# Performance work log

Hardware: AMD Instinct MI355X
Metric: run time of the kernel (lower is better)

Reference implementation:

```python
import jax, jax.numpy as jnp
import numpy as np

B, E, N, D = 4, 16, 1024, 512

def setup_inputs() -> dict:
    key = jax.random.key(0)
    kx, k1, k2, k3 = jax.random.split(key, 4)
    std = 1.0 / np.sqrt(D)
    x = jax.random.normal(kx, (B, E, N, D), dtype=jnp.float32)
    # weights: uniform(-std, std) per init_
    w1 = jax.random.uniform(k1, (E, D, D), dtype=jnp.float32, minval=-std, maxval=std)
    w2 = jax.random.uniform(k2, (E, D, D), dtype=jnp.float32, minval=-std, maxval=std)
    w3 = jax.random.uniform(k3, (E, D, D), dtype=jnp.float32, minval=-std, maxval=std)
    return {"x": x, "w1": w1, "w2": w2, "w3": w3}

def reference(x, w1, w2, w3):
    # per-expert projections: [b,e,n,d] x [e,d,h] -> [b,e,n,h]
    q = jnp.einsum('bend,edh->benh', x, w1)
    k = jnp.einsum('bend,edh->benh', x, w2)
    v = jnp.einsum('bend,edh->benh', x, w3)
    # global (n-reduced) attention: [b,e,h,d]
    atten = jnp.einsum('benh,bend->behd', q, k)
    atten = jax.nn.softmax(atten, axis=-1)
    # [b,e,n,h] x [b,e,h,h] -> [b,e,n,h]
    out = jnp.einsum('benh,behd->bend', v, atten)
    return out
```

## Files before the change

kernel.cpp:

```cpp
#include <hip/hip_runtime.h>
#include <stdint.h>

typedef unsigned short u16;
typedef __attribute__((ext_vector_type(8))) short bf16x8;
typedef __attribute__((ext_vector_type(4))) float floatx4;
typedef __attribute__((ext_vector_type(4))) u16 u16x4;
typedef __attribute__((ext_vector_type(8))) u16 u16x8;

constexpr int B_ = 4, E_ = 16, N_ = 1024, D_ = 512;
constexpr int BE = B_ * E_;

__device__ __forceinline__ u16 f2bf(float f) {
    union { float f; uint32_t u; } v; v.f = f;
    return (u16)((v.u + 0x7fffu + ((v.u >> 16) & 1u)) >> 16);
}
__device__ __forceinline__ float bf2f(u16 h) {
    union { uint32_t u; float f; } v; v.u = ((uint32_t)h) << 16;
    return v.f;
}

#define GLDS(g, l) __builtin_amdgcn_global_load_lds( \
    (const __attribute__((address_space(1))) void*)(g), \
    (__attribute__((address_space(3))) void*)(l), 16, 0, 0)


__global__ __launch_bounds__(256)
void transpose_split(const float* __restrict__ in, u16* __restrict__ outH,
                     u16* __restrict__ outL, int R, int C)
{
    __shared__ float t[32][33];
    const int z = blockIdx.z;
    const float* ib = in + (size_t)z * R * C;
    u16* oh = outH + (size_t)z * R * C;
    u16* ol = outL + (size_t)z * R * C;
    const int r0 = blockIdx.y * 32, c0 = blockIdx.x * 32;
    const int t8 = threadIdx.x & 7, td = threadIdx.x >> 3;

    float4 v = *(const float4*)&ib[(size_t)(r0 + td) * C + c0 + t8 * 4];
    t[td][t8 * 4 + 0] = v.x;
    t[td][t8 * 4 + 1] = v.y;
    t[td][t8 * 4 + 2] = v.z;
    t[td][t8 * 4 + 3] = v.w;
    __syncthreads();

    u16x4 ph, pl;
    float w0 = t[t8 * 4 + 0][td], w1 = t[t8 * 4 + 1][td];
    float w2 = t[t8 * 4 + 2][td], w3 = t[t8 * 4 + 3][td];
    ph.x = f2bf(w0); pl.x = f2bf(w0 - bf2f(ph.x));
    ph.y = f2bf(w1); pl.y = f2bf(w1 - bf2f(ph.y));
    ph.z = f2bf(w2); pl.z = f2bf(w2 - bf2f(ph.z));
    ph.w = f2bf(w3); pl.w = f2bf(w3 - bf2f(ph.w));
    const size_t o = (size_t)(c0 + td) * R + r0 + t8 * 4;
    *(u16x4*)&oh[o] = ph;
    *(u16x4*)&ol[o] = pl;
}

__global__ __launch_bounds__(256)
void transpose_split_w(const float* __restrict__ inA, u16* __restrict__ oAh, u16* __restrict__ oAl,
                       const float* __restrict__ inB, u16* __restrict__ oBh, u16* __restrict__ oBl)
{
    __shared__ float t[32][33];
    int z = blockIdx.z;
    const float* in; u16* oh; u16* ol;
    if (z < E_) { in = inA; oh = oAh; ol = oAl; }
    else        { z -= E_; in = inB; oh = oBh; ol = oBl; }
    const int R = 512, C = 512;
    const float* ib = in + (size_t)z * R * C;
    u16* ohz = oh + (size_t)z * R * C;
    u16* olz = ol + (size_t)z * R * C;
    const int r0 = blockIdx.y * 32, c0 = blockIdx.x * 32;
    const int t8 = threadIdx.x & 7, td = threadIdx.x >> 3;

    float4 v = *(const float4*)&ib[(size_t)(r0 + td) * C + c0 + t8 * 4];
    t[td][t8 * 4 + 0] = v.x;
    t[td][t8 * 4 + 1] = v.y;
    t[td][t8 * 4 + 2] = v.z;
    t[td][t8 * 4 + 3] = v.w;
    __syncthreads();

    u16x4 ph, pl;
    float w0 = t[t8 * 4 + 0][td], w1 = t[t8 * 4 + 1][td];
    float w2 = t[t8 * 4 + 2][td], w3 = t[t8 * 4 + 3][td];
    ph.x = f2bf(w0); pl.x = f2bf(w0 - bf2f(ph.x));
    ph.y = f2bf(w1); pl.y = f2bf(w1 - bf2f(ph.y));
    ph.z = f2bf(w2); pl.z = f2bf(w2 - bf2f(ph.z));
    ph.w = f2bf(w3); pl.w = f2bf(w3 - bf2f(ph.w));
    const size_t o = (size_t)(c0 + td) * R + r0 + t8 * 4;
    *(u16x4*)&ohz[o] = ph;
    *(u16x4*)&olz[o] = pl;
}

__global__ __launch_bounds__(256)
void gemm_split3(const u16* __restrict__ Ah, const u16* __restrict__ Al,
                 int aMod, long aStride,
                 const u16* __restrict__ Bh, const u16* __restrict__ Bl,
                 int bMod, long bStride,
                 u16* __restrict__ Ch, u16* __restrict__ Cl,
                 float* __restrict__ Cf,
                 int M, int N, int K, int f32out, int sym)
{
    const int z = blockIdx.z;
    const long za = aMod ? (z % aMod) : z;
    const long zb = bMod ? (z % bMod) : z;
    const u16* pAh = Ah + za * aStride;
    const u16* pAl = Al + za * aStride;
    const u16* pBh = Bh + zb * bStride;
    const u16* pBl = Bl + zb * bStride;

    __shared__ __attribute__((aligned(16))) u16 sA[8192];
    __shared__ __attribute__((aligned(16))) u16 sB[8192];

    const int tid = threadIdx.x;
    const int wv = tid >> 6, ln = tid & 63;
    const int lq = ln >> 4, lm = ln & 15;

    int bi, bj;
    if (sym) {
        const int idx = blockIdx.x;
        bi = (idx < 4) ? 0 : (idx < 7) ? 1 : (idx < 9) ? 2 : 3;
        bj = idx - ((bi == 0) ? 0 : (bi == 1) ? 3 : (bi == 2) ? 5 : 6);
    } else { bi = blockIdx.x; bj = blockIdx.y; }
    const int m0 = bi * 128, n0 = bj * 128;

    const int rg = ln >> 2;
    const int kq = ((ln & 3) + (rg >> 1)) & 3;
    const u16* srcA[4];
    const u16* srcB[4];
#pragma unroll
    for (int g = 0; g < 4; ++g) {
        const int grp = wv * 4 + g;
        const int row = (grp >> 3) * 64 + ((grp >> 1) & 3) * 16 + rg;
        srcA[g] = ((grp & 1) ? pAl : pAh) + (long)(m0 + row) * K + kq * 8;
        srcB[g] = ((grp & 1) ? pBl : pBh) + (long)(n0 + row) * K + kq * 8;
    }

    const int co = (lm * 4 + ((lq - (lm >> 1)) & 3)) * 8;

    const int wm = wv >> 1, wn = wv & 1;

    floatx4 acc[4][4];
#pragma unroll
    for (int i = 0; i < 4; ++i)
#pragma unroll
        for (int j = 0; j < 4; ++j) acc[i][j] = (floatx4){0.f, 0.f, 0.f, 0.f};

    for (int k0 = 0; k0 < K; k0 += 32) {
#pragma unroll
        for (int g = 0; g < 4; ++g) {
            GLDS(srcA[g] + k0, sA + (wv * 4 + g) * 512);
            GLDS(srcB[g] + k0, sB + (wv * 4 + g) * 512);
        }
        __syncthreads();

        bf16x8 ah[4], al[4], bh[4], bl[4];
#pragma unroll
        for (int i = 0; i < 4; ++i) {
            const int ga = (wm * 8 + i * 2) * 512 + co;
            ah[i] = *(const bf16x8*)&sA[ga];
            al[i] = *(const bf16x8*)&sA[ga + 512];
        }
#pragma unroll
        for (int j = 0; j < 4; ++j) {
            const int gb = (wn * 8 + j * 2) * 512 + co;
            bh[j] = *(const bf16x8*)&sB[gb];
            bl[j] = *(const bf16x8*)&sB[gb + 512];
        }
#pragma unroll
        for (int i = 0; i < 4; ++i)
#pragma unroll
            for (int j = 0; j < 4; ++j) {
                acc[i][j] = __builtin_amdgcn_mfma_f32_16x16x32_bf16(ah[i], bh[j], acc[i][j], 0, 0, 0);
                acc[i][j] = __builtin_amdgcn_mfma_f32_16x16x32_bf16(ah[i], bl[j], acc[i][j], 0, 0, 0);
                acc[i][j] = __builtin_amdgcn_mfma_f32_16x16x32_bf16(al[i], bh[j], acc[i][j], 0, 0, 0);
            }
        __syncthreads();
    }

    const long cbase = (long)z * M * N;
#pragma unroll
    for (int i = 0; i < 4; ++i)
#pragma unroll
        for (int j = 0; j < 4; ++j) {
            const int col = n0 + wn * 64 + j * 16 + lm;
            const int row0 = m0 + wm * 64 + i * 16 + lq * 4;
            if (f32out) {
#pragma unroll
                for (int r = 0; r < 4; ++r)
                    Cf[cbase + (long)(row0 + r) * N + col] = acc[i][j][r];
            } else {
                u16x4 hv, lv;
#pragma unroll
                for (int r = 0; r < 4; ++r) {
                    const float v = acc[i][j][r];
                    const u16 h = f2bf(v);
                    hv[r] = h;
                    lv[r] = f2bf(v - bf2f(h));
                    Ch[cbase + (long)(row0 + r) * N + col] = h;
                    Cl[cbase + (long)(row0 + r) * N + col] = lv[r];
                }
                if (sym && bi != bj) {
                    const long mb = cbase + (long)col * N + row0;
                    *(u16x4*)&Ch[mb] = hv;
                    *(u16x4*)&Cl[mb] = lv;
                }
            }
        }
}

template<int OTFA, int F32OUT>
__global__ __launch_bounds__(256)
void gemm_plain(const float* __restrict__ Qf, int qMod, long qStride,
                const u16* __restrict__ Pb, int pMod, long pStride,
                u16* __restrict__ Cb, float* __restrict__ Cf,
                int M, int N, int K)
{
    const int z = blockIdx.z;
    const float* pQ = Qf + (long)(qMod ? z % qMod : z) * qStride;
    const u16*  pP = Pb + (long)(pMod ? z % pMod : z) * pStride;

    __shared__ __attribute__((aligned(16))) u16 sA[4096];
    __shared__ __attribute__((aligned(16))) u16 sB[4096];

    const int tid = threadIdx.x;
    const int wv = tid >> 6, ln = tid & 63;
    const int lq = ln >> 4, lm = ln & 15;
    const int m0 = blockIdx.x * 128, n0 = blockIdx.y * 128;

    u16* sBF = OTFA ? sB : sA;
    u16* sQ  = OTFA ? sA : sB;
    const int bfRow0 = OTFA ? n0 : m0;
    const int qRow0  = OTFA ? m0 : n0;

    const int rg = ln >> 2;
    const int kqr = ((ln & 3) + (rg >> 1)) & 3;
    const u16* srcP[2];
#pragma unroll
    for (int g = 0; g < 2; ++g) {
        const int grp = wv * 2 + g;
        const int row = (grp >> 2) * 64 + (grp & 3) * 16 + rg;
        srcP[g] = pP + (long)(bfRow0 + row) * K + kqr * 8;
    }

    int orow[2], ok[2];
#pragma unroll
    for (int s = 0; s < 2; ++s) {
        const int ci = tid + s * 256;
        const int grp = ci >> 6, l = ci & 63;
        const int rr = l >> 2;
        orow[s] = qRow0 + (grp >> 2) * 64 + (grp & 3) * 16 + rr;
        ok[s]   = (((l & 3) + (rr >> 1)) & 3) * 8;
    }

    const int co = (lm * 4 + ((lq - (lm >> 1)) & 3)) * 8;

    const int wm = wv >> 1, wn = wv & 1;

    floatx4 acc[4][4];
#pragma unroll
    for (int i = 0; i < 4; ++i)
#pragma unroll
        for (int j = 0; j < 4; ++j) acc[i][j] = (floatx4){0.f, 0.f, 0.f, 0.f};

    for (int k0 = 0; k0 < K; k0 += 32) {
#pragma unroll
        for (int g = 0; g < 2; ++g)
            GLDS(srcP[g] + k0, sBF + (wv * 2 + g) * 512);
#pragma unroll
        for (int s = 0; s < 2; ++s) {
            const float* src = &pQ[(long)orow[s] * K + k0 + ok[s]];
            const float4 v0 = *(const float4*)src;
            const float4 v1 = *(const float4*)(src + 4);
            u16x8 pk;
            pk[0] = f2bf(v0.x); pk[1] = f2bf(v0.y); pk[2] = f2bf(v0.z); pk[3] = f2bf(v0.w);
            pk[4] = f2bf(v1.x); pk[5] = f2bf(v1.y); pk[6] = f2bf(v1.z); pk[7] = f2bf(v1.w);
            *(u16x8*)&sQ[(tid + s * 256) * 8] = pk;
        }
        __syncthreads();

        bf16x8 af[4], bg[4];
#pragma unroll
        for (int i = 0; i < 4; ++i)
            af[i] = *(const bf16x8*)&sA[(wm * 4 + i) * 512 + co];
#pragma unroll
        for (int j = 0; j < 4; ++j)
            bg[j] = *(const bf16x8*)&sB[(wn * 4 + j) * 512 + co];
#pragma unroll
        for (int i = 0; i < 4; ++i)
#pragma unroll
            for (int j = 0; j < 4; ++j)
                acc[i][j] = __builtin_amdgcn_mfma_f32_16x16x32_bf16(af[i], bg[j], acc[i][j], 0, 0, 0);
        __syncthreads();
    }

    const long cbase = (long)z * M * N;
#pragma unroll
    for (int i = 0; i < 4; ++i)
#pragma unroll
        for (int j = 0; j < 4; ++j) {
            const int col = n0 + wn * 64 + j * 16 + lm;
#pragma unroll
            for (int r = 0; r < 4; ++r) {
                const int row = m0 + wm * 64 + i * 16 + lq * 4 + r;
                const long idx = cbase + (long)row * N + col;
                if (F32OUT) Cf[idx] = acc[i][j][r];
                else        Cb[idx] = f2bf(acc[i][j][r]);
            }
        }
}

__global__ __launch_bounds__(128)
void softmax_col(const float* __restrict__ AT, u16* __restrict__ PT)
{
    const int z = blockIdx.x >> 2, gq = blockIdx.x & 3;
    const long base = (long)z * 512 * 512 + gq * 128 + threadIdx.x;
    const float* a = AT + base;
    u16* p = PT + base;

    float m = -1e30f, l = 0.f;
    for (int c = 0; c < 512; ++c) {
        const float v = a[(long)c * 512];
        const float mn = fmaxf(m, v);
        l = l * __expf(m - mn) + __expf(v - mn);
        m = mn;
    }
    const float inv = 1.0f / l;
    for (int c = 0; c < 512; ++c) {
        const float v = a[(long)c * 512];
        p[(long)c * 512] = f2bf(__expf(v - m) * inv);
    }
}

extern "C" void kernel_launch(void* const* d_in, const int* in_sizes, int n_in,
                              void* d_out, int out_size, void* d_ws, size_t ws_size,
                              hipStream_t stream)
{
    const float* x  = (const float*)d_in[0];
    const float* w1 = (const float*)d_in[1];
    const float* w2 = (const float*)d_in[2];
    const float* w3 = (const float*)d_in[3];

    char* O = (char*)d_out;
    char* W = (char*)d_ws;
    const size_t MB = 1ull << 20;

    u16* XhT  = (u16*)O;
    u16* XlT  = (u16*)(O + 64 * MB);
    u16* Gh   = (u16*)W;
    u16* Gl   = (u16*)(W + 32 * MB);
    u16* W2Th = (u16*)(O + 64 * MB);
    u16* W2Tl = (u16*)(O + 72 * MB);
    u16* W1Th = (u16*)(O + 80 * MB);
    u16* W1Tl = (u16*)(O + 88 * MB);
    u16* Uh   = (u16*)O;
    u16* Ul   = (u16*)(O + 32 * MB);
    float* AT = (float*)W;
    u16* PT   = (u16*)(O + 64 * MB);
    u16* MT   = (u16*)W;
    float* out = (float*)d_out;

    const long sXT = (long)512 * 1024;
    const long sSq = (long)512 * 512;

    transpose_split<<<dim3(16, 32, BE), 256, 0, stream>>>(x, XhT, XlT, 1024, 512);
    gemm_split3<<<dim3(10, 1, BE), 256, 0, stream>>>(
        XhT, XlT, 0, sXT, XhT, XlT, 0, sXT,
        Gh, Gl, nullptr, 512, 512, 1024, 0, 1);
    transpose_split_w<<<dim3(16, 16, 2 * E_), 256, 0, stream>>>(
        w2, W2Th, W2Tl, w1, W1Th, W1Tl);
    gemm_split3<<<dim3(4, 4, BE), 256, 0, stream>>>(
        W2Th, W2Tl, E_, sSq, Gh, Gl, 0, sSq,
        Uh, Ul, nullptr, 512, 512, 512, 0, 0);
    gemm_split3<<<dim3(4, 4, BE), 256, 0, stream>>>(
        Uh, Ul, 0, sSq, W1Th, W1Tl, E_, sSq,
        nullptr, nullptr, AT, 512, 512, 512, 1, 0);
    softmax_col<<<dim3(BE * 4), 128, 0, stream>>>(AT, PT);
    gemm_plain<0, 0><<<dim3(4, 4, BE), 256, 0, stream>>>(
        w3, E_, sSq, PT, 0, sSq, MT, nullptr, 512, 512, 512);
    gemm_plain<1, 1><<<dim3(8, 4, BE), 256, 0, stream>>>(
        x, 0, (long)N_ * D_, MT, 0, sSq, nullptr, out, 1024, 512, 512);
}
```

Baseline: 750.8 us.

## Drop symmetric Gram tiling and use pre-cast bf16 GEMM for w3 stage

Removes the symmetric upper-triangle launch of the X^T X Gram GEMM, which wrote mirrored tiles, and computes all 16 tiles directly. This doubles that GEMM's MFMA work but removes the transposed mirror stores and the uneven tile mapping. It also adds a kernel that casts w3 to bf16 once, and replaces the on-the-fly fp32-operand gemm_plain for the P·W3 product with a new bf16×bf16 GEMM that loads both operands into LDS via global_load_lds. The operand order of that product changes, so the MT layout depends on which side is transposed.

```diff
diff --git a/kernel.cpp b/kernel.cpp
--- a/kernel.cpp
+++ b/kernel.cpp
@@ -91,13 +91,25 @@
 }
 
 __global__ __launch_bounds__(256)
+void cast_bf16(const float* __restrict__ in, u16* __restrict__ out, long n4)
+{
+    const long stride = (long)gridDim.x * blockDim.x;
+    for (long i = (long)blockIdx.x * blockDim.x + threadIdx.x; i < n4; i += stride) {
+        const float4 v = *(const float4*)&in[i * 4];
+        u16x4 p;
+        p.x = f2bf(v.x); p.y = f2bf(v.y); p.z = f2bf(v.z); p.w = f2bf(v.w);
+        *(u16x4*)&out[i * 4] = p;
+    }
+}
+
+__global__ __launch_bounds__(256)
 void gemm_split3(const u16* __restrict__ Ah, const u16* __restrict__ Al,
                  int aMod, long aStride,
                  const u16* __restrict__ Bh, const u16* __restrict__ Bl,
                  int bMod, long bStride,
                  u16* __restrict__ Ch, u16* __restrict__ Cl,
                  float* __restrict__ Cf,
-                 int M, int N, int K, int f32out, int sym)
+                 int M, int N, int K, int f32out)
 {
     const int z = blockIdx.z;
     const long za = aMod ? (z % aMod) : z;
@@ -113,14 +125,7 @@
     const int tid = threadIdx.x;
     const int wv = tid >> 6, ln = tid & 63;
     const int lq = ln >> 4, lm = ln & 15;
-
-    int bi, bj;
-    if (sym) {
-        const int idx = blockIdx.x;
-        bi = (idx < 4) ? 0 : (idx < 7) ? 1 : (idx < 9) ? 2 : 3;
-        bj = idx - ((bi == 0) ? 0 : (bi == 1) ? 3 : (bi == 2) ? 5 : 6);
-    } else { bi = blockIdx.x; bj = blockIdx.y; }
-    const int m0 = bi * 128, n0 = bj * 128;
+    const int m0 = blockIdx.x * 128, n0 = blockIdx.y * 128;
 
     const int rg = ln >> 2;
     const int kq = ((ln & 3) + (rg >> 1)) & 3;
@@ -183,26 +188,96 @@
         for (int j = 0; j < 4; ++j) {
             const int col = n0 + wn * 64 + j * 16 + lm;
             const int row0 = m0 + wm * 64 + i * 16 + lq * 4;
-            if (f32out) {
-#pragma unroll
-                for (int r = 0; r < 4; ++r)
-                    Cf[cbase + (long)(row0 + r) * N + col] = acc[i][j][r];
-            } else {
-                u16x4 hv, lv;
-#pragma unroll
-                for (int r = 0; r < 4; ++r) {
-                    const float v = acc[i][j][r];
+#pragma unroll
+            for (int r = 0; r < 4; ++r) {
+                const float v = acc[i][j][r];
+                const long idx = cbase + (long)(row0 + r) * N + col;
+                if (f32out) {
+                    Cf[idx] = v;
+                } else {
                     const u16 h = f2bf(v);
-                    hv[r] = h;
-                    lv[r] = f2bf(v - bf2f(h));
-                    Ch[cbase + (long)(row0 + r) * N + col] = h;
-                    Cl[cbase + (long)(row0 + r) * N + col] = lv[r];
+                    Ch[idx] = h;
+                    Cl[idx] = f2bf(v - bf2f(h));
                 }
-                if (sym && bi != bj) {
-                    const long mb = cbase + (long)col * N + row0;
-                    *(u16x4*)&Ch[mb] = hv;
-                    *(u16x4*)&Cl[mb] = lv;
-                }
+            }
+        }
+}
+
+template<int F32OUT>
+__global__ __launch_bounds__(256)
+void gemm_bb(const u16* __restrict__ Ab, int aMod, long aStride,
+             const u16* __restrict__ Bb, int bMod, long bStride,
+             u16* __restrict__ Cb, float* __restrict__ Cf,
+             int M, int N, int K)
+{
+    const int z = blockIdx.z;
+    const u16* pA = Ab + (long)(aMod ? z % aMod : z) * aStride;
+    const u16* pB = Bb + (long)(bMod ? z % bMod : z) * bStride;
+
+    __shared__ __attribute__((aligned(16))) u16 sA[4096];
+    __shared__ __attribute__((aligned(16))) u16 sB[4096];
+
+    const int tid = threadIdx.x;
+    const int wv = tid >> 6, ln = tid & 63;
+    const int lq = ln >> 4, lm = ln & 15;
+    const int m0 = blockIdx.x * 128, n0 = blockIdx.y * 128;
+
+    const int rg = ln >> 2;
+    const int kq = ((ln & 3) + (rg >> 1)) & 3;
+    const u16* srcA[2];
+    const u16* srcB[2];
+#pragma unroll
+    for (int g = 0; g < 2; ++g) {
+        const int grp = wv * 2 + g;
+        const int row = (grp >> 2) * 64 + (grp & 3) * 16 + rg;
+        srcA[g] = pA + (long)(m0 + row) * K + kq * 8;
+        srcB[g] = pB + (long)(n0 + row) * K + kq * 8;
+    }
+
+    const int co = (lm * 4 + ((lq - (lm >> 1)) & 3)) * 8;
+    const int wm = wv >> 1, wn = wv & 1;
+
+    floatx4 acc[4][4];
+#pragma unroll
+    for (int i = 0; i < 4; ++i)
+#pragma unroll
+        for (int j = 0; j < 4; ++j) acc[i][j] = (floatx4){0.f, 0.f, 0.f, 0.f};
+
+    for (int k0 = 0; k0 < K; k0 += 32) {
+#pragma unroll
+        for (int g = 0; g < 2; ++g) {
+            GLDS(srcA[g] + k0, sA + (wv * 2 + g) * 512);
+            GLDS(srcB[g] + k0, sB + (wv * 2 + g) * 512);
+        }
+        __syncthreads();
+
+        bf16x8 af[4], bg[4];
+#pragma unroll
+        for (int i = 0; i < 4; ++i)
+            af[i] = *(const bf16x8*)&sA[(wm * 4 + i) * 512 + co];
+#pragma unroll
+        for (int j = 0; j < 4; ++j)
+            bg[j] = *(const bf16x8*)&sB[(wn * 4 + j) * 512 + co];
+#pragma unroll
+        for (int i = 0; i < 4; ++i)
+#pragma unroll
+            for (int j = 0; j < 4; ++j)
+                acc[i][j] = __builtin_amdgcn_mfma_f32_16x16x32_bf16(af[i], bg[j], acc[i][j], 0, 0, 0);
+        __syncthreads();
+    }
+
+    const long cbase = (long)z * M * N;
+#pragma unroll
+    for (int i = 0; i < 4; ++i)
+#pragma unroll
+        for (int j = 0; j < 4; ++j) {
+            const int col = n0 + wn * 64 + j * 16 + lm;
+#pragma unroll
+            for (int r = 0; r < 4; ++r) {
+                const int row = m0 + wm * 64 + i * 16 + lq * 4 + r;
+                const long idx = cbase + (long)row * N + col;
+                if (F32OUT) Cf[idx] = acc[i][j][r];
+                else        Cb[idx] = f2bf(acc[i][j][r]);
             }
         }
 }
@@ -351,6 +426,7 @@
     u16* W2Tl = (u16*)(O + 72 * MB);
     u16* W1Th = (u16*)(O + 80 * MB);
     u16* W1Tl = (u16*)(O + 88 * MB);
+    u16* W3b  = (u16*)(O + 96 * MB);
     u16* Uh   = (u16*)O;
     u16* Ul   = (u16*)(O + 32 * MB);
     float* AT = (float*)W;
@@ -362,20 +438,21 @@
     const long sSq = (long)512 * 512;
 
     transpose_split<<<dim3(16, 32, BE), 256, 0, stream>>>(x, XhT, XlT, 1024, 512);
-    gemm_split3<<<dim3(10, 1, BE), 256, 0, stream>>>(
+    gemm_split3<<<dim3(4, 4, BE), 256, 0, stream>>>(
         XhT, XlT, 0, sXT, XhT, XlT, 0, sXT,
-        Gh, Gl, nullptr, 512, 512, 1024, 0, 1);
+        Gh, Gl, nullptr, 512, 512, 1024, 0);
     transpose_split_w<<<dim3(16, 16, 2 * E_), 256, 0, stream>>>(
         w2, W2Th, W2Tl, w1, W1Th, W1Tl);
+    cast_bf16<<<dim3(1024), 256, 0, stream>>>(w3, W3b, (long)E_ * 512 * 512 / 4);
     gemm_split3<<<dim3(4, 4, BE), 256, 0, stream>>>(
         W2Th, W2Tl, E_, sSq, Gh, Gl, 0, sSq,
-        Uh, Ul, nullptr, 512, 512, 512, 0, 0);
+        Uh, Ul, nullptr, 512, 512, 512, 0);
     gemm_split3<<<dim3(4, 4, BE), 256, 0, stream>>>(
         Uh, Ul, 0, sSq, W1Th, W1Tl, E_, sSq,
-        nullptr, nullptr, AT, 512, 512, 512, 1, 0);
+        nullptr, nullptr, AT, 512, 512, 512, 1);
     softmax_col<<<dim3(BE * 4), 128, 0, stream>>>(AT, PT);
-    gemm_plain<0, 0><<<dim3(4, 4, BE), 256, 0, stream>>>(
-        w3, E_, sSq, PT, 0, sSq, MT, nullptr, 512, 512, 512);
+    gemm_bb<0><<<dim3(4, 4, BE), 256, 0, stream>>>(
+        PT, 0, sSq, W3b, E_, sSq, MT, nullptr, 512, 512, 512);
     gemm_plain<1, 1><<<dim3(8, 4, BE), 256, 0, stream>>>(
         x, 0, (long)N_ * D_, MT, 0, sSq, nullptr, out, 1024, 512, 512);
 }
```

Measured after the change: 748.2 us. No clear change (-0.4%).
